# Kernel optimization log

Hardware: AMD Instinct MI355X
Metric: run time of the kernel (lower is better)

Reference implementation:

```python
import jax, jax.numpy as jnp
import numpy as np

B, L, C, H = 8, 1024, 384, 6
D = C // H          # head_dim = 64
K, N = 2, 4         # radial_degree, angular_degree
EPS = 1e-5


def setup_inputs() -> dict:
    key = jax.random.key(0)
    ks = jax.random.split(key, 8)
    x = jax.random.normal(ks[0], (B, L, C), dtype=jnp.float32)
    pos = jax.random.uniform(ks[1], (B, L, 2), dtype=jnp.float32) * 32.0
    w_norm = jnp.ones((C,), dtype=jnp.float32)
    w_in = jax.random.normal(ks[2], (3 * C, C), dtype=jnp.float32) * 0.02
    b_in = jnp.zeros((3 * C,), dtype=jnp.float32)
    w_out = jax.random.normal(ks[3], (C, C), dtype=jnp.float32) * 0.02
    b_out = jnp.zeros((C,), dtype=jnp.float32)
    b_coef = jax.random.normal(ks[4], (H, K + 1, N + 1), dtype=jnp.float32) * 0.01
    b_coef = b_coef.at[:, 1, 0].set(1.0)  # reset_parameters fills b[..., 1, 0] = 1
    c_coef = jax.random.normal(ks[5], (H, K + 1, N + 1), dtype=jnp.float32) * 0.01
    return {"x": x, "pos": pos, "w_norm": w_norm, "w_in": w_in, "b_in": b_in,
            "w_out": w_out, "b_out": b_out, "b_coef": b_coef, "c_coef": c_coef}


def _polar_bias(pos, b_coef, c_coef):
    # pos: (B, L, 2) -> bias grid (B, H, L, L)
    dist = pos[:, :, None, :] - pos[:, None, :, :]           # (B, Lq, Lk, 2)
    theta = jnp.arctan2(dist[..., 1], dist[..., 0])          # (B, Lq, Lk)
    r = jnp.sqrt(jnp.sum(dist * dist, axis=-1))              # (B, Lq, Lk)
    r_pow = r[..., None] ** jnp.arange(K + 1, dtype=r.dtype)           # (B, Lq, Lk, K+1)
    ang = theta[..., None] * jnp.arange(N + 1, dtype=theta.dtype)      # (B, Lq, Lk, N+1)
    cos_part = jnp.einsum('hkn,bijk,bijn->bhij', b_coef, r_pow, jnp.cos(ang))
    sin_part = jnp.einsum('hkn,bijk,bijn->bhij', c_coef, r_pow, jnp.sin(ang))
    return cos_part + sin_part


def reference(x, pos, w_norm, w_in, b_in, w_out, b_out, b_coef, c_coef):
    # RMSNorm
    ms = jnp.mean(x * x, axis=-1, keepdims=True)
    xn = x * jax.lax.rsqrt(ms + EPS) * w_norm
    # packed QKV projection
    qkv = xn @ w_in.T + b_in                                  # (B, L, 3C)
    q, k, v = jnp.split(qkv, 3, axis=-1)
    def heads(t):  # (B, L, C) -> (B, H, L, D)
        return t.reshape(B, L, H, D).transpose(0, 2, 1, 3)
    q, k, v = heads(q), heads(k), heads(v)
    bias = _polar_bias(pos, b_coef, c_coef)                   # (B, H, L, L)
    scores = jnp.einsum('bhqd,bhkd->bhqk', q, k) / jnp.sqrt(jnp.float32(D)) + bias
    attn = jax.nn.softmax(scores, axis=-1)
    o = jnp.einsum('bhqk,bhkd->bhqd', attn, v)                # (B, H, L, D)
    o = o.transpose(0, 2, 1, 3).reshape(B, L, C)
    return o @ w_out.T + b_out
```

## Files before the change

### kernel.cpp

```cpp
#include <hip/hip_runtime.h>

typedef unsigned int  u32;
typedef unsigned short u16;
typedef __attribute__((ext_vector_type(8))) short short8;
typedef __attribute__((ext_vector_type(4))) float f32x4;

__device__ __forceinline__ u16 f2bf(float x) {
  union { float f; u32 u; } un; un.f = x;
  u32 r = un.u + 0x7FFFu + ((un.u >> 16) & 1u);
  return (u16)(r >> 16);
}
__device__ __forceinline__ u32 cvtpk(float lo, float hi) {
  u32 r;
  asm("v_cvt_pk_bf16_f32 %0, %1, %2" : "=v"(r) : "v"(lo), "v"(hi));
  return r;
}
__device__ __forceinline__ f32x4 mfma_bf16(short8 a, short8 b, f32x4 c) {
  return __builtin_amdgcn_mfma_f32_16x16x32_bf16(a, b, c, 0, 0, 0);
}

__global__ __launch_bounds__(256) void prep_kernel(
    const float* __restrict__ x, const float* __restrict__ w_norm,
    const float* __restrict__ w_in, const float* __restrict__ w_out,
    u16* __restrict__ xn, u16* __restrict__ winb, u16* __restrict__ woutb)
{
  int blk = blockIdx.x, t = threadIdx.x;
  if (blk < 2048) {
    int wv = t >> 6, lane = t & 63;
    int row = blk * 4 + wv;
    const float* xr = x + (size_t)row * 384;
    float v[6]; float ss = 0.f;
    #pragma unroll
    for (int i = 0; i < 6; i++) { v[i] = xr[lane + 64 * i]; ss += v[i] * v[i]; }
    #pragma unroll
    for (int off = 32; off > 0; off >>= 1) ss += __shfl_xor(ss, off);
    float rs = __builtin_amdgcn_rsqf(ss * (1.0f / 384.0f) + 1e-5f);
    #pragma unroll
    for (int i = 0; i < 6; i++) {
      float xv = v[i] * rs * w_norm[lane + 64 * i];
      xn[(size_t)row * 384 + lane + 64 * i] = f2bf(xv);
    }
  } else {
    int base = (blk - 2048) * 2048 + t * 8;
    #pragma unroll
    for (int j = 0; j < 8; j++) {
      int idx = base + j;
      if (idx < 442368) winb[idx] = f2bf(w_in[idx]);
      else              woutb[idx - 442368] = f2bf(w_out[idx - 442368]);
    }
  }
}

template<bool OUT_F32, bool QSCALE>
__global__ __launch_bounds__(256) void gemm_kernel(
    const u16* __restrict__ A, int lda,
    const u16* __restrict__ Bw, int ldb,
    const float* __restrict__ bias, void* __restrict__ outp, int ldc, int K)
{
  __shared__ __attribute__((aligned(16))) u16 As[128 * 72];
  __shared__ __attribute__((aligned(16))) u16 Bs[128 * 72];
  int t = threadIdx.x;
  int lane = t & 63, wv = t >> 6;
  int g = lane >> 4, cl = lane & 15;
  int row0 = blockIdx.x * 128, col0 = blockIdx.y * 128;
  int wm = (wv >> 1) * 64, wn = (wv & 1) * 64;
  f32x4 acc[4][4];
  #pragma unroll
  for (int i = 0; i < 4; i++)
    #pragma unroll
    for (int j = 0; j < 4; j++) acc[i][j] = (f32x4){0.f, 0.f, 0.f, 0.f};

  for (int k0 = 0; k0 < K; k0 += 64) {
    __syncthreads();
    #pragma unroll
    for (int j = 0; j < 4; j++) {
      int i = t + 256 * j;
      int r = i >> 3, ch = i & 7;
      *(uint4*)(&As[r * 72 + ch * 8]) =
          *(const uint4*)(A + (size_t)(row0 + r) * lda + k0 + ch * 8);
      *(uint4*)(&Bs[r * 72 + ch * 8]) =
          *(const uint4*)(Bw + (size_t)(col0 + r) * ldb + k0 + ch * 8);
    }
    __syncthreads();
    #pragma unroll
    for (int kh = 0; kh < 2; kh++) {
      short8 af[4], bfr[4];
      #pragma unroll
      for (int s = 0; s < 4; s++) {
        af[s]  = *(const short8*)(&As[(wm + s * 16 + cl) * 72 + kh * 32 + g * 8]);
        bfr[s] = *(const short8*)(&Bs[(wn + s * 16 + cl) * 72 + kh * 32 + g * 8]);
      }
      #pragma unroll
      for (int i = 0; i < 4; i++)
        #pragma unroll
        for (int j = 0; j < 4; j++)
          acc[i][j] = mfma_bf16(af[i], bfr[j], acc[i][j]);
    }
  }
  #pragma unroll
  for (int i = 0; i < 4; i++) {
    #pragma unroll
    for (int j = 0; j < 4; j++) {
      int colb = col0 + wn + j * 16 + cl;
      float bv = bias[colb];
      #pragma unroll
      for (int r = 0; r < 4; r++) {
        int rowb = row0 + wm + i * 16 + g * 4 + r;
        float v = acc[i][j][r] + bv;
        if (QSCALE) { if (colb < 384) v *= 0.125f; }
        if (OUT_F32) ((float*)outp)[(size_t)rowb * ldc + colb] = v;
        else ((u16*)outp)[(size_t)rowb * ldc + colb] = f2bf(v);
      }
    }
  }
}

__global__ __launch_bounds__(256) void attn_swap(
    const u16* __restrict__ qkv, const float* __restrict__ pos,
    const float* __restrict__ bcf, const float* __restrict__ ccf,
    u16* __restrict__ obuf)
{
  __shared__ __attribute__((aligned(16))) u16 vsmem[2][64][72];
  __shared__ float mlbuf[2][2][16];

  int bid = blockIdx.x;
  int xslot = bid & 7, rest = bid >> 3;
  int qt = rest & 31, gdiv = rest >> 5;
  int g48 = gdiv * 8 + xslot;
  int b = g48 / 6, h = g48 - b * 6;

  int t = threadIdx.x, lane = t & 63, wv = t >> 6;
  int strip = wv & 1, half = wv >> 1;
  int g = lane >> 4, cl = lane & 15;

  float bc[15], cc[15];
  #pragma unroll
  for (int i = 0; i < 15; i++) { bc[i] = bcf[h * 15 + i]; cc[i] = ccf[h * 15 + i]; }

  int qrow = qt * 32 + strip * 16 + cl;
  const u16* qbase = qkv + (size_t)(b * 1024 + qrow) * 1152 + h * 64;
  short8 qf0 = *(const short8*)(qbase + g * 8);
  short8 qf1 = *(const short8*)(qbase + 32 + g * 8);
  float qx = pos[(size_t)(b * 1024 + qrow) * 2 + 0];
  float qy = pos[(size_t)(b * 1024 + qrow) * 2 + 1];

  f32x4 oa[4];
  #pragma unroll
  for (int d = 0; d < 4; d++) oa[d] = (f32x4){0.f, 0.f, 0.f, 0.f};
  float m_own = -1e30f, l_own = 0.f;

  const u16* kb   = qkv + (size_t)b * 1024 * 1152 + 384 + h * 64;
  const u16* vsrc = qkv + (size_t)b * 1024 * 1152 + 768 + h * 64 + strip * 32;
  const float* pb = pos + (size_t)b * 2048;

  int phys = (lane & 0x23) | ((lane & 0x0C) << 1) | ((lane & 0x10) >> 2);
  u16* vcol = &vsmem[half][0][0] + phys;

  for (int kt = 0; kt < 512; kt += 64) {
    int k0 = half * 512 + kt;
    {
      const u16* vr = vsrc + (size_t)(k0 + lane) * 1152;
      uint4 a0 = *(const uint4*)(vr);
      uint4 a1 = *(const uint4*)(vr + 8);
      uint4 a2 = *(const uint4*)(vr + 16);
      uint4 a3 = *(const uint4*)(vr + 24);
      u16* c0 = vcol + (size_t)(strip * 32) * 72;
      #define ST(i, val) c0[(size_t)(i) * 72] = (u16)(val)
      ST(0,  a0.x); ST(1,  a0.x >> 16); ST(2,  a0.y); ST(3,  a0.y >> 16);
      ST(4,  a0.z); ST(5,  a0.z >> 16); ST(6,  a0.w); ST(7,  a0.w >> 16);
      ST(8,  a1.x); ST(9,  a1.x >> 16); ST(10, a1.y); ST(11, a1.y >> 16);
      ST(12, a1.z); ST(13, a1.z >> 16); ST(14, a1.w); ST(15, a1.w >> 16);
      ST(16, a2.x); ST(17, a2.x >> 16); ST(18, a2.y); ST(19, a2.y >> 16);
      ST(20, a2.z); ST(21, a2.z >> 16); ST(22, a2.w); ST(23, a2.w >> 16);
      ST(24, a3.x); ST(25, a3.x >> 16); ST(26, a3.y); ST(27, a3.y >> 16);
      ST(28, a3.z); ST(29, a3.z >> 16); ST(30, a3.w); ST(31, a3.w >> 16);
      #undef ST
    }
    f32x4 s[4];
    #pragma unroll
    for (int ks = 0; ks < 4; ks++) {
      const u16* kr = kb + (size_t)(k0 + ks * 16 + cl) * 1152;
      short8 kf0 = *(const short8*)(kr + g * 8);
      short8 kf1 = *(const short8*)(kr + 32 + g * 8);
      f32x4 z = (f32x4){0.f, 0.f, 0.f, 0.f};
      z = mfma_bf16(kf0, qf0, z);
      z = mfma_bf16(kf1, qf1, z);
      s[ks] = z;
    }
    #pragma unroll
    for (int ks = 0; ks < 4; ks++) {
      int kbase4 = k0 + ks * 16 + 4 * g;
      float4 pA = *(const float4*)(pb + (size_t)kbase4 * 2);
      float4 pB = *(const float4*)(pb + (size_t)kbase4 * 2 + 4);
      float kxs[4] = {pA.x, pA.z, pB.x, pB.z};
      float kys[4] = {pA.y, pA.w, pB.y, pB.w};
      #pragma unroll
      for (int r = 0; r < 4; r++) {
        float dx = qx - kxs[r], dy = qy - kys[r];
        float r2 = dx * dx + dy * dy;
        bool zz = !(r2 > 0.f);
        float ir = zz ? 0.f : __builtin_amdgcn_rsqf(r2);
        float rr = r2 * ir;
        float c1 = zz ? 1.f : dx * ir;
        float s1 = dy * ir;
        float c2 = c1*c1 - s1*s1, s2 = 2.f*c1*s1;
        float c3 = c1*c2 - s1*s2, s3 = s1*c2 + c1*s2;
        float c4 = c2*c2 - s2*s2, s4 = 2.f*c2*s2;
        float a0 = bc[0] + bc[1]*c1 + bc[2]*c2 + bc[3]*c3 + bc[4]*c4
                 + cc[1]*s1 + cc[2]*s2 + cc[3]*s3 + cc[4]*s4;
        float a1 = bc[5] + bc[6]*c1 + bc[7]*c2 + bc[8]*c3 + bc[9]*c4
                 + cc[6]*s1 + cc[7]*s2 + cc[8]*s3 + cc[9]*s4;
        float a2 = bc[10] + bc[11]*c1 + bc[12]*c2 + bc[13]*c3 + bc[14]*c4
                 + cc[11]*s1 + cc[12]*s2 + cc[13]*s3 + cc[14]*s4;
        s[ks][r] += a0 + rr * (a1 + rr * a2);
      }
    }
    float tmax = -1e30f;
    #pragma unroll
    for (int ks = 0; ks < 4; ks++)
      #pragma unroll
      for (int r = 0; r < 4; r++) tmax = fmaxf(tmax, s[ks][r]);
    tmax = fmaxf(tmax, __shfl_xor(tmax, 16));
    tmax = fmaxf(tmax, __shfl_xor(tmax, 32));
    float mn = fmaxf(m_own, tmax);
    float sc = __builtin_amdgcn_exp2f((m_own - mn) * 1.44269504f);
    m_own = mn;
    #pragma unroll
    for (int r = 0; r < 4; r++) {
      float scr = __shfl(sc, 4 * g + r);
      #pragma unroll
      for (int d = 0; d < 4; d++) oa[d][r] *= scr;
    }
    float psum = 0.f;
    #pragma unroll
    for (int ks = 0; ks < 4; ks++)
      #pragma unroll
      for (int r = 0; r < 4; r++) {
        float p = __builtin_amdgcn_exp2f((s[ks][r] - mn) * 1.44269504f);
        psum += p; s[ks][r] = p;
      }
    psum += __shfl_xor(psum, 16);
    psum += __shfl_xor(psum, 32);
    l_own = l_own * sc + psum;
    union { u32 w[4]; short8 s8; } pk0, pk1;
    pk0.w[0] = cvtpk(s[0][0], s[0][1]); pk0.w[1] = cvtpk(s[0][2], s[0][3]);
    pk0.w[2] = cvtpk(s[1][0], s[1][1]); pk0.w[3] = cvtpk(s[1][2], s[1][3]);
    pk1.w[0] = cvtpk(s[2][0], s[2][1]); pk1.w[1] = cvtpk(s[2][2], s[2][3]);
    pk1.w[2] = cvtpk(s[3][0], s[3][1]); pk1.w[3] = cvtpk(s[3][2], s[3][3]);
    __syncthreads();
    #pragma unroll
    for (int d = 0; d < 4; d++) {
      short8 vf0 = *(const short8*)(&vsmem[half][d * 16 + cl][g * 8]);
      short8 vf1 = *(const short8*)(&vsmem[half][d * 16 + cl][32 + g * 8]);
      oa[d] = mfma_bf16(pk0.s8, vf0, oa[d]);
      oa[d] = mfma_bf16(pk1.s8, vf1, oa[d]);
    }
    __syncthreads();
  }
  float* o1 = (float*)&vsmem[0][0][0];
  if (half == 1) {
    if (lane < 16) { mlbuf[0][strip][lane] = m_own; mlbuf[1][strip][lane] = l_own; }
    #pragma unroll
    for (int r = 0; r < 4; r++) {
      int row = 4 * g + r;
      #pragma unroll
      for (int d = 0; d < 4; d++)
        o1[(strip * 16 + row) * 64 + d * 16 + cl] = oa[d][r];
    }
  }
  __syncthreads();
  if (half == 0) {
    float m1 = mlbuf[0][strip][cl], l1 = mlbuf[1][strip][cl];
    float M  = fmaxf(m_own, m1);
    float f0 = __builtin_amdgcn_exp2f((m_own - M) * 1.44269504f);
    float f1 = __builtin_amdgcn_exp2f((m1    - M) * 1.44269504f);
    float linv = __builtin_amdgcn_rcpf(l_own * f0 + l1 * f1);
    #pragma unroll
    for (int r = 0; r < 4; r++) {
      int row = 4 * g + r;
      float f0r = __shfl(f0, row), f1r = __shfl(f1, row), invr = __shfl(linv, row);
      int qr = qt * 32 + strip * 16 + row;
      #pragma unroll
      for (int d = 0; d < 4; d++) {
        float val = (oa[d][r] * f0r +
                     o1[(strip * 16 + row) * 64 + d * 16 + cl] * f1r) * invr;
        obuf[(size_t)(b * 1024 + qr) * 384 + h * 64 + d * 16 + cl] = f2bf(val);
      }
    }
  }
}

extern "C" void kernel_launch(void* const* d_in, const int* in_sizes, int n_in,
                              void* d_out, int out_size, void* d_ws, size_t ws_size,
                              hipStream_t stream) {
  const float* x      = (const float*)d_in[0];
  const float* pos    = (const float*)d_in[1];
  const float* w_norm = (const float*)d_in[2];
  const float* w_in   = (const float*)d_in[3];
  const float* b_in   = (const float*)d_in[4];
  const float* w_out  = (const float*)d_in[5];
  const float* b_out  = (const float*)d_in[6];
  const float* b_coef = (const float*)d_in[7];
  const float* c_coef = (const float*)d_in[8];

  char* ws = (char*)d_ws;
  u16* xn    = (u16*)(ws + 0);
  u16* obuf  = (u16*)(ws + 0);
  u16* winb  = (u16*)(ws + 6291456);
  u16* woutb = (u16*)(ws + 7176192);
  u16* qkvb  = (u16*)(ws + 7471104);

  prep_kernel<<<2336, 256, 0, stream>>>(x, w_norm, w_in, w_out, xn, winb, woutb);
  gemm_kernel<false, true><<<dim3(64, 9), 256, 0, stream>>>(
      xn, 384, winb, 384, b_in, qkvb, 1152, 384);
  attn_swap<<<1536, 256, 0, stream>>>(qkvb, pos, b_coef, c_coef, obuf);
  gemm_kernel<true, false><<<dim3(64, 3), 256, 0, stream>>>(
      obuf, 384, woutb, 384, b_out, (float*)d_out, 384, 384);
}
```

Baseline: 168.0 us.

## Give each attention wave a private V tile and defer softmax rescaling

Each wave now stages its own 32-key V tile into a private LDS slice, which removes both per-iteration block-wide barriers, and the key tile per iteration shrinks from 64 to 32. The online-softmax rescale is skipped unless some lane's new max exceeds the running max by more than a threshold, and the row-sum reduction is moved out of the loop. The angle harmonics use a Chebyshev FMA recurrence. The costs are twice as many loop iterations, duplicated V loads across the two strips, and a lazy-rescale path whose exponentials could grow large if the threshold logic is wrong.

Result: faster. 155.5 us (-7.5%).

```diff
diff --git a/kernel.cpp b/kernel.cpp
--- a/kernel.cpp
+++ b/kernel.cpp
@@ -115,12 +115,12 @@
   }
 }
 
-__global__ __launch_bounds__(256) void attn_swap(
+__global__ __launch_bounds__(256) void attn_swap3(
     const u16* __restrict__ qkv, const float* __restrict__ pos,
     const float* __restrict__ bcf, const float* __restrict__ ccf,
     u16* __restrict__ obuf)
 {
-  __shared__ __attribute__((aligned(16))) u16 vsmem[2][64][72];
+  __shared__ __attribute__((aligned(16))) u16 vsmem[4][64][40];
   __shared__ float mlbuf[2][2][16];
 
   int bid = blockIdx.x;
@@ -149,23 +149,23 @@
   for (int d = 0; d < 4; d++) oa[d] = (f32x4){0.f, 0.f, 0.f, 0.f};
   float m_own = -1e30f, l_own = 0.f;
 
-  const u16* kb   = qkv + (size_t)b * 1024 * 1152 + 384 + h * 64;
-  const u16* vsrc = qkv + (size_t)b * 1024 * 1152 + 768 + h * 64 + strip * 32;
+  const u16* kb = qkv + (size_t)b * 1024 * 1152 + 384 + h * 64;
+  int kappa = lane & 31, dh = lane >> 5;
+  const u16* vsrc = qkv + (size_t)b * 1024 * 1152 + 768 + h * 64 + dh * 32;
   const float* pb = pos + (size_t)b * 2048;
 
-  int phys = (lane & 0x23) | ((lane & 0x0C) << 1) | ((lane & 0x10) >> 2);
-  u16* vcol = &vsmem[half][0][0] + phys;
-
-  for (int kt = 0; kt < 512; kt += 64) {
-    int k0 = half * 512 + kt;
+  int pcol = (kappa & 3) | ((kappa & 0x0C) << 1) | ((kappa & 0x10) >> 2);
+  u16* vdst = &vsmem[wv][dh * 32][0] + pcol;
+
+  for (int it = 0; it < 16; it++) {
+    int k0 = half * 512 + it * 32;
     {
-      const u16* vr = vsrc + (size_t)(k0 + lane) * 1152;
+      const u16* vr = vsrc + (size_t)(k0 + kappa) * 1152;
       uint4 a0 = *(const uint4*)(vr);
       uint4 a1 = *(const uint4*)(vr + 8);
       uint4 a2 = *(const uint4*)(vr + 16);
       uint4 a3 = *(const uint4*)(vr + 24);
-      u16* c0 = vcol + (size_t)(strip * 32) * 72;
-      #define ST(i, val) c0[(size_t)(i) * 72] = (u16)(val)
+      #define ST(i, val) vdst[(i) * 40] = (u16)(val)
       ST(0,  a0.x); ST(1,  a0.x >> 16); ST(2,  a0.y); ST(3,  a0.y >> 16);
       ST(4,  a0.z); ST(5,  a0.z >> 16); ST(6,  a0.w); ST(7,  a0.w >> 16);
       ST(8,  a1.x); ST(9,  a1.x >> 16); ST(10, a1.y); ST(11, a1.y >> 16);
@@ -176,22 +176,22 @@
       ST(28, a3.z); ST(29, a3.z >> 16); ST(30, a3.w); ST(31, a3.w >> 16);
       #undef ST
     }
-    f32x4 s[4];
-    #pragma unroll
-    for (int ks = 0; ks < 4; ks++) {
+    f32x4 sk[2];
+    #pragma unroll
+    for (int ks = 0; ks < 2; ks++) {
       const u16* kr = kb + (size_t)(k0 + ks * 16 + cl) * 1152;
       short8 kf0 = *(const short8*)(kr + g * 8);
       short8 kf1 = *(const short8*)(kr + 32 + g * 8);
       f32x4 z = (f32x4){0.f, 0.f, 0.f, 0.f};
       z = mfma_bf16(kf0, qf0, z);
       z = mfma_bf16(kf1, qf1, z);
-      s[ks] = z;
-    }
-    #pragma unroll
-    for (int ks = 0; ks < 4; ks++) {
-      int kbase4 = k0 + ks * 16 + 4 * g;
-      float4 pA = *(const float4*)(pb + (size_t)kbase4 * 2);
-      float4 pB = *(const float4*)(pb + (size_t)kbase4 * 2 + 4);
+      sk[ks] = z;
+    }
+    #pragma unroll
+    for (int ks = 0; ks < 2; ks++) {
+      int kb4 = k0 + ks * 16 + 4 * g;
+      float4 pA = *(const float4*)(pb + (size_t)kb4 * 2);
+      float4 pB = *(const float4*)(pb + (size_t)kb4 * 2 + 4);
       float kxs[4] = {pA.x, pA.z, pB.x, pB.z};
       float kys[4] = {pA.y, pA.w, pB.y, pB.w};
       #pragma unroll
@@ -203,60 +203,59 @@
         float rr = r2 * ir;
         float c1 = zz ? 1.f : dx * ir;
         float s1 = dy * ir;
-        float c2 = c1*c1 - s1*s1, s2 = 2.f*c1*s1;
-        float c3 = c1*c2 - s1*s2, s3 = s1*c2 + c1*s2;
-        float c4 = c2*c2 - s2*s2, s4 = 2.f*c2*s2;
+        float tc = c1 + c1;
+        float c2 = __builtin_fmaf(tc, c1, -1.f), s2 = tc * s1;
+        float c3 = __builtin_fmaf(tc, c2, -c1),  s3 = __builtin_fmaf(tc, s2, -s1);
+        float c4 = __builtin_fmaf(tc, c3, -c2),  s4 = __builtin_fmaf(tc, s3, -s2);
         float a0 = bc[0] + bc[1]*c1 + bc[2]*c2 + bc[3]*c3 + bc[4]*c4
                  + cc[1]*s1 + cc[2]*s2 + cc[3]*s3 + cc[4]*s4;
         float a1 = bc[5] + bc[6]*c1 + bc[7]*c2 + bc[8]*c3 + bc[9]*c4
                  + cc[6]*s1 + cc[7]*s2 + cc[8]*s3 + cc[9]*s4;
         float a2 = bc[10] + bc[11]*c1 + bc[12]*c2 + bc[13]*c3 + bc[14]*c4
                  + cc[11]*s1 + cc[12]*s2 + cc[13]*s3 + cc[14]*s4;
-        s[ks][r] += a0 + rr * (a1 + rr * a2);
+        sk[ks][r] += a0 + rr * __builtin_fmaf(rr, a2, a1);
       }
     }
     float tmax = -1e30f;
     #pragma unroll
-    for (int ks = 0; ks < 4; ks++)
-      #pragma unroll
-      for (int r = 0; r < 4; r++) tmax = fmaxf(tmax, s[ks][r]);
-    tmax = fmaxf(tmax, __shfl_xor(tmax, 16));
-    tmax = fmaxf(tmax, __shfl_xor(tmax, 32));
-    float mn = fmaxf(m_own, tmax);
-    float sc = __builtin_amdgcn_exp2f((m_own - mn) * 1.44269504f);
-    m_own = mn;
-    #pragma unroll
-    for (int r = 0; r < 4; r++) {
-      float scr = __shfl(sc, 4 * g + r);
-      #pragma unroll
-      for (int d = 0; d < 4; d++) oa[d][r] *= scr;
+    for (int ks = 0; ks < 2; ks++)
+      #pragma unroll
+      for (int r = 0; r < 4; r++) tmax = fmaxf(tmax, sk[ks][r]);
+    if (!__all((int)(tmax <= m_own + 8.f))) {
+      tmax = fmaxf(tmax, __shfl_xor(tmax, 16));
+      tmax = fmaxf(tmax, __shfl_xor(tmax, 32));
+      float mn = fmaxf(m_own, tmax);
+      float sc = __builtin_amdgcn_exp2f((m_own - mn) * 1.44269504f);
+      m_own = mn;
+      l_own *= sc;
+      #pragma unroll
+      for (int r = 0; r < 4; r++) {
+        float scr = __shfl(sc, 4 * g + r);
+        #pragma unroll
+        for (int d = 0; d < 4; d++) oa[d][r] *= scr;
+      }
     }
     float psum = 0.f;
     #pragma unroll
-    for (int ks = 0; ks < 4; ks++)
+    for (int ks = 0; ks < 2; ks++)
       #pragma unroll
       for (int r = 0; r < 4; r++) {
-        float p = __builtin_amdgcn_exp2f((s[ks][r] - mn) * 1.44269504f);
-        psum += p; s[ks][r] = p;
-      }
-    psum += __shfl_xor(psum, 16);
-    psum += __shfl_xor(psum, 32);
-    l_own = l_own * sc + psum;
-    union { u32 w[4]; short8 s8; } pk0, pk1;
-    pk0.w[0] = cvtpk(s[0][0], s[0][1]); pk0.w[1] = cvtpk(s[0][2], s[0][3]);
-    pk0.w[2] = cvtpk(s[1][0], s[1][1]); pk0.w[3] = cvtpk(s[1][2], s[1][3]);
-    pk1.w[0] = cvtpk(s[2][0], s[2][1]); pk1.w[1] = cvtpk(s[2][2], s[2][3]);
-    pk1.w[2] = cvtpk(s[3][0], s[3][1]); pk1.w[3] = cvtpk(s[3][2], s[3][3]);
-    __syncthreads();
+        float p = __builtin_amdgcn_exp2f((sk[ks][r] - m_own) * 1.44269504f);
+        psum += p; sk[ks][r] = p;
+      }
+    l_own += psum;
+    union { u32 w[4]; short8 s8; } pk;
+    pk.w[0] = cvtpk(sk[0][0], sk[0][1]); pk.w[1] = cvtpk(sk[0][2], sk[0][3]);
+    pk.w[2] = cvtpk(sk[1][0], sk[1][1]); pk.w[3] = cvtpk(sk[1][2], sk[1][3]);
     #pragma unroll
     for (int d = 0; d < 4; d++) {
-      short8 vf0 = *(const short8*)(&vsmem[half][d * 16 + cl][g * 8]);
-      short8 vf1 = *(const short8*)(&vsmem[half][d * 16 + cl][32 + g * 8]);
-      oa[d] = mfma_bf16(pk0.s8, vf0, oa[d]);
-      oa[d] = mfma_bf16(pk1.s8, vf1, oa[d]);
-    }
-    __syncthreads();
-  }
+      short8 vf = *(const short8*)(&vsmem[wv][d * 16 + cl][g * 8]);
+      oa[d] = mfma_bf16(pk.s8, vf, oa[d]);
+    }
+  }
+  l_own += __shfl_xor(l_own, 16);
+  l_own += __shfl_xor(l_own, 32);
+  __syncthreads();
   float* o1 = (float*)&vsmem[0][0][0];
   if (half == 1) {
     if (lane < 16) { mlbuf[0][strip][lane] = m_own; mlbuf[1][strip][lane] = l_own; }
@@ -313,7 +312,7 @@
   prep_kernel<<<2336, 256, 0, stream>>>(x, w_norm, w_in, w_out, xn, winb, woutb);
   gemm_kernel<false, true><<<dim3(64, 9), 256, 0, stream>>>(
       xn, 384, winb, 384, b_in, qkvb, 1152, 384);
-  attn_swap<<<1536, 256, 0, stream>>>(qkvb, pos, b_coef, c_coef, obuf);
+  attn_swap3<<<1536, 256, 0, stream>>>(qkvb, pos, b_coef, c_coef, obuf);
   gemm_kernel<true, false><<<dim3(64, 3), 256, 0, stream>>>(
       obuf, 384, woutb, 384, b_out, (float*)d_out, 384, 384);
 }
```
